# Performance work log

Hardware: AMD Instinct MI355X
Metric: run time of the kernel (lower is better)

## Reference

```python
import jax, jax.numpy as jnp
import numpy as np

SOFTENING = 1e-6
EPS = 1e-9
CUTOFF = 0.1
K_NEG = 4
MARGIN = 1.0
KE_FACTOR = 1e-3


def setup_inputs() -> dict:
    key = jax.random.key(0)
    ks = jax.random.split(key, 16)
    B, S, D8, W = 4, 2048, 8, 16
    N = B * S
    return {
        "positions_2d": jax.random.normal(ks[0], (B, S, 2), dtype=jnp.float32),
        "masses": jax.random.uniform(ks[1], (B, S, 1), dtype=jnp.float32),
        "vel_2d": jax.random.normal(ks[2], (N, 2), dtype=jnp.float32),
        "pos_8d": jax.random.normal(ks[3], (N, D8), dtype=jnp.float32),
        "pos_pos_2d": jax.random.normal(ks[4], (N, 2), dtype=jnp.float32),
        "pos_pos_8d": jax.random.normal(ks[5], (N, D8), dtype=jnp.float32),
        "positive_masses": jax.random.uniform(ks[6], (N, 1), dtype=jnp.float32),
        "neg_pos_2d": jax.random.normal(ks[7], (N * K_NEG, 2), dtype=jnp.float32),
        "neg_pos_8d": jax.random.normal(ks[8], (N * K_NEG, D8), dtype=jnp.float32),
        "neg_masses": jax.random.uniform(ks[9], (N * K_NEG, 1), dtype=jnp.float32),
        "exp_masses": jax.random.uniform(ks[10], (N * K_NEG, 1), dtype=jnp.float32),
        "G": jnp.float32(1.0),
        "repulsion_strength": jnp.float32(0.5),
        "well_centers": jax.random.normal(ks[11], (W, D8), dtype=jnp.float32),
        "well_strength": jnp.float32(0.1),
        "temperature": jnp.float32(1.0),
        "entropy_coeff": jnp.float32(0.01),
    }


def _calculate_forces(positions_2d, masses, G, repulsion_strength):
    # positions_2d: [B,S,2], masses: [B,S,1]
    B, S, _ = positions_2d.shape
    # diff[b,i,j] = pos[b,j] - pos[b,i]  -> [B,S,S,2]
    diff = positions_2d[:, None, :, :] - positions_2d[:, :, None, :]
    dist_sq = jnp.sum(diff * diff, axis=-1) + SOFTENING  # [B,S,S]
    dist = jnp.sqrt(dist_sq)
    diag = jnp.eye(S, dtype=bool)  # [S,S], broadcasts over B
    dist_safe = jnp.where(diag, 1.0, dist)
    dist_sq_safe = jnp.where(diag, 1.0, dist_sq)
    mm = masses[:, :, None, 0] * masses[:, None, :, 0]  # [B,S,S]
    attractive = jax.nn.relu(G) * mm / dist_sq_safe
    rep_strength = jax.nn.relu(repulsion_strength)
    repulsive = rep_strength * jax.nn.relu(1.0 - dist_safe / CUTOFF) / (dist_sq_safe * dist_safe + EPS)
    total_mag = repulsive - attractive  # [B,S,S]
    force_vectors = total_mag[..., None] * diff / (dist_safe[..., None] + EPS)
    return jnp.sum(force_vectors, axis=2)  # [B,S,2]


def _cdist(a, b):
    # Euclidean cdist: [N,D] x [W,D] -> [N,W]; W=16 so dense is cheap
    d = a[:, None, :] - b[None, :, :]
    return jnp.sqrt(jnp.sum(d * d, axis=-1))


def _grand_unifying_loss(pos_2d, vel_2d, pos_8d, masses_flat, pos_pos_2d, pos_pos_8d,
                         positive_masses, neg_pos_2d, neg_pos_8d, neg_masses, exp_masses,
                         G, well_centers, well_strength, temperature, entropy_coeff):
    Gp = jax.nn.relu(G)
    dist_pos_2d = jnp.linalg.norm(pos_2d - pos_pos_2d, axis=-1) + EPS  # [N]
    pe_pairwise_pos = -Gp * (masses_flat * positive_masses)[:, 0] / dist_pos_2d
    pos_2d_rep = jnp.repeat(pos_2d, K_NEG, axis=0)  # [N*K,2]
    dist_neg_2d = jnp.linalg.norm(pos_2d_rep - neg_pos_2d, axis=-1) + EPS
    pe_pairwise_neg = -Gp * (exp_masses * neg_masses)[:, 0] / dist_neg_2d

    ws = jax.nn.relu(well_strength)
    all_pos_8d = jnp.concatenate([pos_8d, pos_pos_8d], axis=0)  # [2N,8]
    min_dist_pos = jnp.min(_cdist(all_pos_8d, well_centers), axis=1)
    pe_well_pos = ws * min_dist_pos ** 2
    all_neg_8d = jnp.concatenate([jnp.repeat(pos_8d, K_NEG, axis=0), neg_pos_8d], axis=0)
    min_dist_neg = jnp.min(_cdist(all_neg_8d, well_centers), axis=1)
    pe_well_neg = ws * min_dist_neg ** 2

    U_pos = jnp.mean(pe_pairwise_pos) + jnp.mean(pe_well_pos)
    U_neg = jnp.mean(pe_pairwise_neg) + jnp.mean(pe_well_neg)
    batch_variance = jnp.mean(jnp.var(all_pos_8d, axis=0, ddof=1))  # torch.var is unbiased
    entropy_term = jax.nn.relu(temperature) * jax.nn.relu(entropy_coeff) * batch_variance
    F_pos = U_pos - entropy_term
    F_neg = U_neg - entropy_term
    free_energy_loss = jax.nn.relu(MARGIN + F_pos - F_neg)
    # Original: mean(masses[N,1] * ke[N]) broadcasts to an [N,N] outer product;
    # mean of the outer product == mean(m) * mean(ke) (same value and gradients)
    ke = jnp.sum(vel_2d * vel_2d, axis=-1)  # [N]
    ke_loss = KE_FACTOR * 0.5 * jnp.mean(masses_flat) * jnp.mean(ke)
    return free_energy_loss + ke_loss


def reference(positions_2d, masses, vel_2d, pos_8d, pos_pos_2d, pos_pos_8d,
              positive_masses, neg_pos_2d, neg_pos_8d, neg_masses, exp_masses,
              G, repulsion_strength, well_centers, well_strength, temperature, entropy_coeff):
    forces = _calculate_forces(positions_2d, masses, G, repulsion_strength)
    pos_flat = positions_2d.reshape(-1, 2)
    masses_flat = masses.reshape(-1, 1)
    loss = _grand_unifying_loss(pos_flat, vel_2d, pos_8d, masses_flat, pos_pos_2d,
                                pos_pos_8d, positive_masses, neg_pos_2d, neg_pos_8d,
                                neg_masses, exp_masses, G, well_centers, well_strength,
                                temperature, entropy_coeff)
    return forces, loss
```

## Files before the change

kernel.cpp:

```cpp
#include <hip/hip_runtime.h>

#define SEQ    2048
#define N_PTS  8192
#define NK     32768
#define N2     16384
#define NACC   22
#define NLOSSBLK 256
#define SLOT_DOUBLES (NLOSSBLK * NACC)
#define CTR_OFFSET   (SLOT_DOUBLES * 8)

__device__ __forceinline__ float frcp(float x)  { return __builtin_amdgcn_rcpf(x); }
__device__ __forceinline__ float fsqrt_(float x){ return __builtin_amdgcn_sqrtf(x); }

__device__ __forceinline__ float min_dist2(float4 a, float4 b, const float* __restrict__ wc)
{
    float best = 3.4e38f;
    #pragma unroll
    for (int w = 0; w < 16; ++w) {
        const float* c = &wc[w * 8];
        float d, s;
        d = a.x - c[0]; s = d * d;
        d = a.y - c[1]; s = fmaf(d, d, s);
        d = a.z - c[2]; s = fmaf(d, d, s);
        d = a.w - c[3]; s = fmaf(d, d, s);
        d = b.x - c[4]; s = fmaf(d, d, s);
        d = b.y - c[5]; s = fmaf(d, d, s);
        d = b.z - c[6]; s = fmaf(d, d, s);
        d = b.w - c[7]; s = fmaf(d, d, s);
        best = fminf(best, s);
    }
    return best;
}

__global__ __launch_bounds__(256) void fused_kernel(
    const float* __restrict__ pos,
    const float* __restrict__ mass,
    const float* __restrict__ vel,
    const float* __restrict__ pos8,
    const float* __restrict__ pp2,
    const float* __restrict__ pp8,
    const float* __restrict__ pmass,
    const float* __restrict__ negp2,
    const float* __restrict__ negp8,
    const float* __restrict__ negm,
    const float* __restrict__ expm,
    const float* __restrict__ Gptr,
    const float* __restrict__ Rptr,
    const float* __restrict__ wellc,
    const float* __restrict__ wstr,
    const float* __restrict__ tPtr,
    const float* __restrict__ ecPtr,
    float* __restrict__ out,
    double* __restrict__ slots,
    unsigned int* __restrict__ ctr)
{
    const int tid = threadIdx.x;
    const int blk = blockIdx.x;

    if (blk < 256) {
        __shared__ float sx[SEQ], sy[SEQ], sm[SEQ];
        __shared__ float rf[2][8][32];

        const int b  = blk >> 6;
        const int it = blk & 63;
        const int rowbase = b * SEQ;

        const float2* p2 = (const float2*)pos;
        for (int k = tid; k < SEQ; k += 256) {
            const float2 v = p2[rowbase + k];
            sx[k] = v.x; sy[k] = v.y;
            sm[k] = mass[rowbase + k];
        }
        const float Gv = fmaxf(Gptr[0], 0.0f);
        const float Rv = fmaxf(Rptr[0], 0.0f);
        __syncthreads();

        const int il = tid & 31;
        const int js = tid >> 5;
        const int iloc = it * 32 + il;
        const float px = sx[iloc];
        const float py = sy[iloc];
        const float ci = Gv * sm[iloc];

        float fx = 0.0f, fy = 0.0f;
        const int j0 = js * 256;
        #pragma unroll 4
        for (int jj = 0; jj < 256; ++jj) {
            const int j = j0 + jj;
            const float dx = sx[j] - px;
            const float dy = sy[j] - py;
            const float r2 = fmaf(dx, dx, fmaf(dy, dy, 1e-6f));
            const float r  = fsqrt_(r2);
            const float rp = r + 1e-9f;
            float mor = -(ci * sm[j]) * frcp(r2 * rp);
            const float t = fmaf(-10.0f, r, 1.0f);
            if (t > 0.0f) {
                mor += (Rv * t) * frcp(fmaf(r2, r, 1e-9f) * rp);
            }
            fx = fmaf(mor, dx, fx);
            fy = fmaf(mor, dy, fy);
        }
        rf[0][js][il] = fx;
        rf[1][js][il] = fy;
        __syncthreads();
        if (tid < 64) {
            const int comp = tid >> 5, i2 = tid & 31;
            float s = 0.0f;
            #pragma unroll
            for (int q = 0; q < 8; ++q) s += rf[comp][q][i2];
            out[(rowbase + it * 32 + i2) * 2 + comp] = s;
        }
        return;
    }

    __shared__ float  wc[128];
    __shared__ double red[4][NACC];
    __shared__ int    lastflag;

    if (tid < 128) wc[tid] = wellc[tid];
    if (tid == 0)  lastflag = 0;
    __syncthreads();

    const int lb  = blk - 256;
    const int idx = lb * 256 + tid;

    double acc[NACC];
    #pragma unroll
    for (int k = 0; k < NACC; ++k) acc[k] = 0.0;

    {
        const float* row = (idx < NK) ? (pos8 + (idx >> 2) * 8)
                                      : (negp8 + (idx - NK) * 8);
        const float4 a = ((const float4*)row)[0];
        const float4 b = ((const float4*)row)[1];
        acc[3] = (double)min_dist2(a, b, wc);
    }
    if (idx < NK) {
        const int i = idx >> 2;
        const float dx = pos[i * 2 + 0] - negp2[idx * 2 + 0];
        const float dy = pos[i * 2 + 1] - negp2[idx * 2 + 1];
        const float d  = fsqrt_(fmaf(dx, dx, dy * dy)) + 1e-9f;
        acc[1] = (double)(expm[idx] * negm[idx] / d);
    }
    if (idx < N2) {
        const float* row = (idx < N_PTS) ? (pos8 + idx * 8)
                                         : (pp8 + (idx - N_PTS) * 8);
        const float4 a = ((const float4*)row)[0];
        const float4 b = ((const float4*)row)[1];
        acc[2] = (double)min_dist2(a, b, wc);
        acc[4]  = (double)a.x;  acc[12] = (double)(a.x * a.x);
        acc[5]  = (double)a.y;  acc[13] = (double)(a.y * a.y);
        acc[6]  = (double)a.z;  acc[14] = (double)(a.z * a.z);
        acc[7]  = (double)a.w;  acc[15] = (double)(a.w * a.w);
        acc[8]  = (double)b.x;  acc[16] = (double)(b.x * b.x);
        acc[9]  = (double)b.y;  acc[17] = (double)(b.y * b.y);
        acc[10] = (double)b.z;  acc[18] = (double)(b.z * b.z);
        acc[11] = (double)b.w;  acc[19] = (double)(b.w * b.w);
    }
    if (idx < N_PTS) {
        const float dx = pos[idx * 2 + 0] - pp2[idx * 2 + 0];
        const float dy = pos[idx * 2 + 1] - pp2[idx * 2 + 1];
        const float d  = fsqrt_(fmaf(dx, dx, dy * dy)) + 1e-9f;
        acc[0]  = (double)(mass[idx] * pmass[idx] / d);
        acc[20] = (double)mass[idx];
        const float vx = vel[idx * 2 + 0];
        const float vy = vel[idx * 2 + 1];
        acc[21] = (double)fmaf(vx, vx, vy * vy);
    }

    const int lane = tid & 63, wid = tid >> 6;
    #pragma unroll
    for (int k = 0; k < NACC; ++k) {
        double v = acc[k];
        for (int off = 32; off > 0; off >>= 1) v += __shfl_down(v, off, 64);
        if (lane == 0) red[wid][k] = v;
    }
    __syncthreads();
    if (tid < NACC) {
        slots[lb * NACC + tid] = red[0][tid] + red[1][tid] + red[2][tid] + red[3][tid];
    }
    __syncthreads();
    if (tid == 0) {
        __threadfence();
        const unsigned int ticket = atomicAdd(ctr, 1u);
        if (ticket == NLOSSBLK - 1) lastflag = 1;
    }
    __syncthreads();
    if (!lastflag) return;

    __threadfence();
    #pragma unroll
    for (int k = 0; k < NACC; ++k) {
        double v = slots[tid * NACC + k];
        for (int off = 32; off > 0; off >>= 1) v += __shfl_down(v, off, 64);
        if (lane == 0) red[wid][k] = v;
    }
    __syncthreads();
    if (tid == 0) {
        double s[NACC];
        #pragma unroll
        for (int k = 0; k < NACC; ++k)
            s[k] = red[0][k] + red[1][k] + red[2][k] + red[3][k];

        const double Gp  = fmax((double)Gptr[0], 0.0);
        const double wsp = fmax((double)wstr[0], 0.0);
        const double T   = fmax((double)tPtr[0], 0.0);
        const double ec  = fmax((double)ecPtr[0], 0.0);
        const double Nd = 8192.0, NKd = 32768.0, N2d = 16384.0, NK2d = 65536.0;

        const double U_pos = -Gp * s[0] / Nd  + wsp * s[2] / N2d;
        const double U_neg = -Gp * s[1] / NKd + wsp * s[3] / NK2d;

        double var = 0.0;
        for (int d = 0; d < 8; ++d) {
            const double sx_ = s[4 + d], sxx = s[12 + d];
            var += (sxx - sx_ * sx_ / N2d) / (N2d - 1.0);
        }
        var *= 0.125;
        const double ent = T * ec * var;
        const double Fp = U_pos - ent, Fn = U_neg - ent;
        double fel = 1.0 + Fp - Fn;
        if (fel < 0.0) fel = 0.0;
        const double ke_loss = 1e-3 * 0.5 * (s[20] / Nd) * (s[21] / Nd);
        out[16384] = (float)(fel + ke_loss);
    }
}

extern "C" void kernel_launch(void* const* d_in, const int* in_sizes, int n_in,
                              void* d_out, int out_size, void* d_ws, size_t ws_size,
                              hipStream_t stream)
{
    const float* pos   = (const float*)d_in[0];
    const float* mass  = (const float*)d_in[1];
    const float* vel   = (const float*)d_in[2];
    const float* pos8  = (const float*)d_in[3];
    const float* pp2   = (const float*)d_in[4];
    const float* pp8   = (const float*)d_in[5];
    const float* pmass = (const float*)d_in[6];
    const float* negp2 = (const float*)d_in[7];
    const float* negp8 = (const float*)d_in[8];
    const float* negm  = (const float*)d_in[9];
    const float* expm  = (const float*)d_in[10];
    const float* Gp    = (const float*)d_in[11];
    const float* Rp    = (const float*)d_in[12];
    const float* wellc = (const float*)d_in[13];
    const float* wstr  = (const float*)d_in[14];
    const float* temp  = (const float*)d_in[15];
    const float* ecoef = (const float*)d_in[16];

    float*        out   = (float*)d_out;
    double*       slots = (double*)d_ws;
    unsigned int* ctr   = (unsigned int*)((char*)d_ws + CTR_OFFSET);

    hipMemsetAsync(ctr, 0, sizeof(unsigned int), stream);

    fused_kernel<<<512, 256, 0, stream>>>(pos, mass, vel, pos8, pp2, pp8, pmass,
                                          negp2, negp8, negm, expm, Gp, Rp,
                                          wellc, wstr, temp, ecoef,
                                          out, slots, ctr);
}
```

Baseline: 107.6 us.

## Register-block 4 rows per thread in pairwise force loop, branchless repulsion

The pairwise force kernel now gives each thread 4 i-rows and strides j across 32 lanes, so every shared-memory j load (position packed as float2 plus mass) is reused across 4 rows. The repulsion branch is replaced by a clamped fmax so no lanes diverge, at the cost of always computing the second reciprocal. The partial-sum buffer grows to 32 slices, padded to avoid bank conflicts. The loss path swaps two divisions for hardware reciprocals, which slightly changes precision.

```diff
diff --git a/kernel.cpp b/kernel.cpp
--- a/kernel.cpp
+++ b/kernel.cpp
@@ -58,57 +58,72 @@
     const int blk = blockIdx.x;
 
     if (blk < 256) {
-        __shared__ float sx[SEQ], sy[SEQ], sm[SEQ];
-        __shared__ float rf[2][8][32];
+        __shared__ float2 sxy[SEQ];
+        __shared__ float  sm[SEQ];
+        __shared__ float  rf[2][32][33];
 
         const int b  = blk >> 6;
         const int it = blk & 63;
         const int rowbase = b * SEQ;
 
         const float2* p2 = (const float2*)pos;
-        for (int k = tid; k < SEQ; k += 256) {
-            const float2 v = p2[rowbase + k];
-            sx[k] = v.x; sy[k] = v.y;
-            sm[k] = mass[rowbase + k];
+        #pragma unroll
+        for (int k0 = 0; k0 < SEQ; k0 += 256) {
+            const int k = k0 + tid;
+            sxy[k] = p2[rowbase + k];
+            sm[k]  = mass[rowbase + k];
         }
         const float Gv = fmaxf(Gptr[0], 0.0f);
         const float Rv = fmaxf(Rptr[0], 0.0f);
         __syncthreads();
 
-        const int il = tid & 31;
-        const int js = tid >> 5;
-        const int iloc = it * 32 + il;
-        const float px = sx[iloc];
-        const float py = sy[iloc];
-        const float ci = Gv * sm[iloc];
-
-        float fx = 0.0f, fy = 0.0f;
-        const int j0 = js * 256;
+        const int ig = tid >> 5;
+        const int js = tid & 31;
+        const int i0 = ig * 4;
+
+        float px[4], py[4], ci[4];
+        float fx[4] = {0.f, 0.f, 0.f, 0.f};
+        float fy[4] = {0.f, 0.f, 0.f, 0.f};
+        #pragma unroll
+        for (int s = 0; s < 4; ++s) {
+            const int iloc = it * 32 + i0 + s;
+            px[s] = sxy[iloc].x;
+            py[s] = sxy[iloc].y;
+            ci[s] = Gv * sm[iloc];
+        }
+
         #pragma unroll 4
-        for (int jj = 0; jj < 256; ++jj) {
-            const int j = j0 + jj;
-            const float dx = sx[j] - px;
-            const float dy = sy[j] - py;
-            const float r2 = fmaf(dx, dx, fmaf(dy, dy, 1e-6f));
-            const float r  = fsqrt_(r2);
-            const float rp = r + 1e-9f;
-            float mor = -(ci * sm[j]) * frcp(r2 * rp);
-            const float t = fmaf(-10.0f, r, 1.0f);
-            if (t > 0.0f) {
-                mor += (Rv * t) * frcp(fmaf(r2, r, 1e-9f) * rp);
+        for (int jj = 0; jj < 64; ++jj) {
+            const int j = jj * 32 + js;
+            const float2 pj = sxy[j];
+            const float  mj = sm[j];
+            #pragma unroll
+            for (int s = 0; s < 4; ++s) {
+                const float dx = pj.x - px[s];
+                const float dy = pj.y - py[s];
+                const float r2 = fmaf(dx, dx, fmaf(dy, dy, 1e-6f));
+                const float r  = fsqrt_(r2);
+                const float rp = r + 1e-9f;
+                const float tpos = fmaxf(fmaf(-10.0f, r, 1.0f), 0.0f);
+                const float mor = (Rv * tpos) * frcp(fmaf(r2, r, 1e-9f) * rp)
+                                - (ci[s] * mj) * frcp(r2 * rp);
+                fx[s] = fmaf(mor, dx, fx[s]);
+                fy[s] = fmaf(mor, dy, fy[s]);
             }
-            fx = fmaf(mor, dx, fx);
-            fy = fmaf(mor, dy, fy);
-        }
-        rf[0][js][il] = fx;
-        rf[1][js][il] = fy;
+        }
+
+        #pragma unroll
+        for (int s = 0; s < 4; ++s) {
+            rf[0][js][i0 + s] = fx[s];
+            rf[1][js][i0 + s] = fy[s];
+        }
         __syncthreads();
         if (tid < 64) {
-            const int comp = tid >> 5, i2 = tid & 31;
-            float s = 0.0f;
+            const int c = tid >> 5, i = tid & 31;
+            float sum = 0.f;
             #pragma unroll
-            for (int q = 0; q < 8; ++q) s += rf[comp][q][i2];
-            out[(rowbase + it * 32 + i2) * 2 + comp] = s;
+            for (int q = 0; q < 32; ++q) sum += rf[c][q][i];
+            out[(rowbase + it * 32 + i) * 2 + c] = sum;
         }
         return;
     }
@@ -140,7 +155,7 @@
         const float dx = pos[i * 2 + 0] - negp2[idx * 2 + 0];
         const float dy = pos[i * 2 + 1] - negp2[idx * 2 + 1];
         const float d  = fsqrt_(fmaf(dx, dx, dy * dy)) + 1e-9f;
-        acc[1] = (double)(expm[idx] * negm[idx] / d);
+        acc[1] = (double)(expm[idx] * negm[idx] * frcp(d));
     }
     if (idx < N2) {
         const float* row = (idx < N_PTS) ? (pos8 + idx * 8)
@@ -161,7 +176,7 @@
         const float dx = pos[idx * 2 + 0] - pp2[idx * 2 + 0];
         const float dy = pos[idx * 2 + 1] - pp2[idx * 2 + 1];
         const float d  = fsqrt_(fmaf(dx, dx, dy * dy)) + 1e-9f;
-        acc[0]  = (double)(mass[idx] * pmass[idx] / d);
+        acc[0]  = (double)(mass[idx] * pmass[idx] * frcp(d));
         acc[20] = (double)mass[idx];
         const float vx = vel[idx * 2 + 0];
         const float vy = vel[idx * 2 + 1];
```

Result: slower. 111.8 us (+3.9%).
